# Performance work log

Hardware: AMD Instinct MI355X
Metric: run time of the kernel (lower is better)

Reference implementation:

```python
import jax, jax.numpy as jnp
import numpy as np

H = 8      # heads
D = 64     # dim_head
N0 = 1024  # modality-0 tokens
N1 = 1024  # modality-1 tokens
N = N0 + N1  # == token_num
DI = H * D   # dim_inner = 512


def setup_inputs() -> dict:
    key = jax.random.key(0)
    ks = jax.random.split(key, 10)
    s = 0.02
    return {
        "x0": jax.random.normal(ks[0], (1, N0, 512), jnp.float32),
        "x1": jax.random.normal(ks[1], (1, N1, 512), jnp.float32),
        "mask0": jnp.ones((1, N0), jnp.bool_),
        "mask1": jnp.ones((1, N1), jnp.bool_),
        "attn_dist": jax.random.normal(ks[2], (1, N, N), jnp.float32),
        "W_in0": jax.random.normal(ks[3], (512, 3 * DI), jnp.float32) * s,
        "W_in1": jax.random.normal(ks[4], (512, 3 * DI), jnp.float32) * s,
        "W_tau": jax.random.normal(ks[5], (DI, N * H), jnp.float32) * s,
        "b_tau": jax.random.normal(ks[6], (N * H,), jnp.float32) * s,
        "W_out0": jax.random.normal(ks[7], (DI, 512), jnp.float32) * s,
        "W_out1": jax.random.normal(ks[8], (DI, 512), jnp.float32) * s,
    }


def _split_heads(qkv, B, n):
    # (B, n, 3*H*D) -> (3, B, H, n, D)   [matches Rearrange 'b n (qkv h d) -> qkv b h n d']
    return qkv.reshape(B, n, 3, H, D).transpose(2, 0, 3, 1, 4)


def reference(x0, x1, mask0, mask1, attn_dist, W_in0, W_in1, W_tau, b_tau, W_out0, W_out1):
    B = x0.shape[0]
    qkv0 = _split_heads(x0 @ W_in0, B, N0)
    qkv1 = _split_heads(x1 @ W_in1, B, N1)
    qkv = jnp.concatenate([qkv0, qkv1], axis=3)  # pack along token axis -> (3,B,H,N,D)
    q, k, v = qkv[0], qkv[1], qkv[2]
    mask = jnp.concatenate([mask0, mask1], axis=1)  # (B, N)

    sim = jnp.einsum('bhid,bhjd->bhij', q, k) / jnp.sqrt(jnp.array(D, q.dtype))
    neg = -jnp.finfo(sim.dtype).max
    sim = jnp.where(mask[:, None, None, :], sim, neg)

    # taus: raw row-major reshape of q (B,H,N,D) -> (B,N,H*D), as in torch .reshape
    q_flat = q.reshape(B, N, H * D)
    taus = (q_flat @ W_tau + b_tau).reshape(B, N, N, H)
    bias = (taus * attn_dist[..., None]).transpose(0, 3, 1, 2)  # (B,H,N,N)
    sim = sim - bias

    attn = jax.nn.softmax(sim.astype(jnp.float32), axis=-1).astype(sim.dtype)
    out = jnp.einsum('bhij,bhjd->bhid', attn, v)
    out = out.transpose(0, 2, 1, 3).reshape(B, N, H * D)  # merge heads

    out0 = out[:, :N0] @ W_out0
    out1 = out[:, N0:] @ W_out1
    return (out0, out1)
```

## Files before the change

kernel.cpp:

```cpp
#include <hip/hip_runtime.h>
#include <stdint.h>

typedef __bf16 bf16;
typedef __bf16 bf16x8 __attribute__((ext_vector_type(8)));
typedef float f32x4 __attribute__((ext_vector_type(4)));
typedef unsigned short u16x8 __attribute__((ext_vector_type(8)));

#define MFMA16(a, b, c) __builtin_amdgcn_mfma_f32_16x16x32_bf16(a, b, c, 0, 0, 0)

static __device__ __forceinline__ bf16x8 lds_frag(const unsigned short* p) {
  return __builtin_bit_cast(bf16x8, *(const u16x8*)p);
}

static __device__ __forceinline__ u16x8 cvt8(const float* p) {
  f32x4 a = *(const f32x4*)p;
  f32x4 b = *(const f32x4*)(p + 4);
  u16x8 r;
#pragma unroll
  for (int e = 0; e < 4; ++e) {
    r[e] = __builtin_bit_cast(unsigned short, (bf16)a[e]);
    r[4 + e] = __builtin_bit_cast(unsigned short, (bf16)b[e]);
  }
  return r;
}

__global__ __launch_bounds__(256) void prep_kernel(
    const float* __restrict__ Wti, const float* __restrict__ btau,
    const float* __restrict__ x0, const float* __restrict__ x1,
    const float* __restrict__ Win0, const float* __restrict__ Win1,
    const float* __restrict__ Wo0, const float* __restrict__ Wo1,
    bf16* __restrict__ Wto, float* __restrict__ bto, bf16* __restrict__ xb,
    bf16* __restrict__ Winb0, bf16* __restrict__ Winb1,
    bf16* __restrict__ Wob0, bf16* __restrict__ Wob1) {
  const int b = blockIdx.x;
  const int tid = threadIdx.x;
  __shared__ unsigned short shm[8 * 32 * 72];

  if (b < 512) {
    const int c0 = (b & 7) * 64;
    const int j0 = (b >> 3) * 32;
#pragma unroll
    for (int it = 0; it < 8; ++it) {
      int idx = it * 256 + tid;
      int c = idx >> 5, j = idx & 31;
      u16x8 v = cvt8(Wti + (size_t)(c0 + c) * 16384 + (j0 + j) * 8);
#pragma unroll
      for (int h = 0; h < 8; ++h) shm[(h * 32 + j) * 72 + c] = v[h];
    }
    __syncthreads();
#pragma unroll
    for (int it = 0; it < 8; ++it) {
      int chunk = it * 256 + tid;
      int row = chunk >> 3, ck = chunk & 7;
      int h = row >> 5, j = row & 31;
      u16x8 v = *(const u16x8*)&shm[row * 72 + ck * 8];
      *(u16x8*)((unsigned short*)Wto + (size_t)(h * 2048 + j0 + j) * 512 + c0 + ck * 8) = v;
    }
    if ((b & 7) == 0) {
      int j = tid >> 3, h = tid & 7;
      bto[h * 2048 + j0 + j] = btau[(j0 + j) * 8 + h];
    }
  } else if (b < 896) {
    int t = b - 512;
    const float* W = t < 192 ? Win0 : Win1;
    bf16* Wb = t < 192 ? Winb0 : Winb1;
    t = t < 192 ? t : t - 192;
    const int c0 = (t & 7) * 64, n0 = (t >> 3) * 64;
#pragma unroll
    for (int it = 0; it < 2; ++it) {
      int idx = it * 256 + tid;
      int c = idx >> 3, nn = idx & 7;
      u16x8 v = cvt8(W + (size_t)(c0 + c) * 1536 + n0 + nn * 8);
#pragma unroll
      for (int e = 0; e < 8; ++e) shm[(nn * 8 + e) * 72 + c] = v[e];
    }
    __syncthreads();
#pragma unroll
    for (int it = 0; it < 2; ++it) {
      int idx = it * 256 + tid;
      int n = idx >> 3, ck = idx & 7;
      *(u16x8*)((unsigned short*)Wb + (size_t)(n0 + n) * 512 + c0 + ck * 8) =
          *(const u16x8*)&shm[n * 72 + ck * 8];
    }
  } else if (b < 1408) {
    int t = b - 896;
    const float* src = t < 256 ? x0 : x1;
    size_t dst0 = t < 256 ? 0 : 524288;
    int tt = t < 256 ? t : t - 256;
    size_t off = (size_t)tt * 2048 + tid * 8;
    u16x8 v = cvt8(src + off);
    *(u16x8*)((unsigned short*)xb + dst0 + off) = v;
  } else {
    int t = b - 1408;
    const float* W = t < 64 ? Wo0 : Wo1;
    bf16* Wb = t < 64 ? Wob0 : Wob1;
    t &= 63;
    const int c0 = (t & 7) * 64, n0 = (t >> 3) * 64;
#pragma unroll
    for (int it = 0; it < 2; ++it) {
      int idx = it * 256 + tid;
      int c = idx >> 3, nn = idx & 7;
      u16x8 v = cvt8(W + (size_t)(c0 + c) * 512 + n0 + nn * 8);
#pragma unroll
      for (int e = 0; e < 8; ++e) shm[(nn * 8 + e) * 72 + c] = v[e];
    }
    __syncthreads();
#pragma unroll
    for (int it = 0; it < 2; ++it) {
      int idx = it * 256 + tid;
      int n = idx >> 3, ck = idx & 7;
      *(u16x8*)((unsigned short*)Wb + (size_t)(n0 + n) * 512 + c0 + ck * 8) =
          *(const u16x8*)&shm[n * 72 + ck * 8];
    }
  }
}

__global__ __launch_bounds__(256) void qkv_gemm(
    const bf16* __restrict__ xb, const bf16* __restrict__ Winb0, const bf16* __restrict__ Winb1,
    bf16* __restrict__ Qb, bf16* __restrict__ Kb, bf16* __restrict__ Vb) {
  const int i0 = blockIdx.x * 128, c0 = blockIdx.y * 128;
  const bf16* Bm = (i0 < 1024) ? Winb0 : Winb1;
  const int tid = threadIdx.x;
  const int lane = tid & 63, wave = tid >> 6;
  const int l16 = lane & 15, quad = lane >> 4;
  const int mrow = (wave & 1) * 64, ncol = (wave >> 1) * 64;
  __shared__ unsigned short As[128 * 64];
  __shared__ unsigned short Bs[128 * 64];
  f32x4 acc[4][4] = {};

  for (int k0 = 0; k0 < 512; k0 += 64) {
    __syncthreads();
#pragma unroll
    for (int c = 0; c < 4; ++c) {
      int s = c * 256 + tid;
      int row = s >> 3, pos = s & 7;
      int kc = pos ^ (row & 7);
      __builtin_amdgcn_global_load_lds((const unsigned int*)(xb + (size_t)(i0 + row) * 512 + k0 + kc * 8),
                                       (unsigned int*)&As[s * 8], 16, 0, 0);
      __builtin_amdgcn_global_load_lds((const unsigned int*)(Bm + (size_t)(c0 + row) * 512 + k0 + kc * 8),
                                       (unsigned int*)&Bs[s * 8], 16, 0, 0);
    }
    __syncthreads();
#pragma unroll
    for (int kb = 0; kb < 2; ++kb) {
      bf16x8 a[4], b[4];
#pragma unroll
      for (int mt = 0; mt < 4; ++mt) {
        int row = mrow + mt * 16 + l16;
        a[mt] = lds_frag(&As[row * 64 + (((kb * 4 + quad) ^ (row & 7)) * 8)]);
      }
#pragma unroll
      for (int nt = 0; nt < 4; ++nt) {
        int row = ncol + nt * 16 + l16;
        b[nt] = lds_frag(&Bs[row * 64 + (((kb * 4 + quad) ^ (row & 7)) * 8)]);
      }
#pragma unroll
      for (int mt = 0; mt < 4; ++mt)
#pragma unroll
        for (int nt = 0; nt < 4; ++nt) acc[mt][nt] = MFMA16(a[mt], b[nt], acc[mt][nt]);
    }
  }
#pragma unroll
  for (int mt = 0; mt < 4; ++mt)
#pragma unroll
    for (int nt = 0; nt < 4; ++nt)
#pragma unroll
      for (int r = 0; r < 4; ++r) {
        int row = i0 + mrow + mt * 16 + quad * 4 + r;
        int col = c0 + ncol + nt * 16 + l16;
        int qsel = col >> 9, h = (col >> 6) & 7, d = col & 63;
        bf16* dst = qsel == 0 ? Qb : (qsel == 1 ? Kb : Vb);
        dst[(size_t)(h * 2048 + row) * 64 + d] = (bf16)acc[mt][nt][r];
      }
}

__global__ __launch_bounds__(256) void tau_gemm(
    const bf16* __restrict__ Qb, const bf16* __restrict__ Wt,
    const float* __restrict__ bt, const float* __restrict__ ad, bf16* __restrict__ T) {
  const int i0 = blockIdx.x * 128;
  const int j0 = blockIdx.y * 16;
  const int tid = threadIdx.x;
  const int lane = tid & 63, wave = tid >> 6;
  const int l16 = lane & 15, quad = lane >> 4;
  const int mrow = (wave & 1) * 64, ncol = (wave >> 1) * 64;
  __shared__ unsigned short As[128 * 128];
  __shared__ unsigned short Bs[128 * 128];
  f32x4 acc[4][4] = {};

  for (int k0 = 0; k0 < 512; k0 += 128) {
    __syncthreads();
#pragma unroll
    for (int c = 0; c < 8; ++c) {
      int s = c * 256 + tid;
      int row = s >> 4, pos = s & 15;
      int kc = pos ^ (row & 7);
      __builtin_amdgcn_global_load_lds((const unsigned int*)(Qb + (size_t)(i0 + row) * 512 + k0 + kc * 8),
                                       (unsigned int*)&As[s * 8], 16, 0, 0);
      __builtin_amdgcn_global_load_lds(
          (const unsigned int*)(Wt + (size_t)((row >> 4) * 2048 + j0 + (row & 15)) * 512 + k0 + kc * 8),
          (unsigned int*)&Bs[s * 8], 16, 0, 0);
    }
    __syncthreads();
#pragma unroll
    for (int kb = 0; kb < 4; ++kb) {
      bf16x8 a[4], b[4];
#pragma unroll
      for (int mt = 0; mt < 4; ++mt) {
        int row = mrow + mt * 16 + l16;
        a[mt] = lds_frag(&As[row * 128 + (((kb * 4 + quad) ^ (row & 7)) * 8)]);
      }
#pragma unroll
      for (int nt = 0; nt < 4; ++nt) {
        int row = ncol + nt * 16 + l16;
        b[nt] = lds_frag(&Bs[row * 128 + (((kb * 4 + quad) ^ (row & 7)) * 8)]);
      }
#pragma unroll
      for (int mt = 0; mt < 4; ++mt)
#pragma unroll
        for (int nt = 0; nt < 4; ++nt) acc[mt][nt] = MFMA16(a[mt], b[nt], acc[mt][nt]);
    }
  }
  float btv[4];
  int hh[4];
#pragma unroll
  for (int nt = 0; nt < 4; ++nt) {
    int c = ncol + nt * 16 + l16;
    hh[nt] = c >> 4;
    btv[nt] = bt[hh[nt] * 2048 + j0 + l16];
  }
#pragma unroll
  for (int mt = 0; mt < 4; ++mt)
#pragma unroll
    for (int r = 0; r < 4; ++r) {
      int row = i0 + mrow + mt * 16 + quad * 4 + r;
      float av = ad[(size_t)row * 2048 + j0 + l16];
#pragma unroll
      for (int nt = 0; nt < 4; ++nt)
        T[(size_t)hh[nt] * 4194304 + (size_t)row * 2048 + j0 + l16] =
            (bf16)((acc[mt][nt][r] + btv[nt]) * av);
    }
}

__global__ __launch_bounds__(256) void attn_kernel(
    const bf16* __restrict__ Qb, const bf16* __restrict__ Kb, const bf16* __restrict__ Vb,
    const bf16* __restrict__ T, float* __restrict__ Op, float* __restrict__ Ml) {
  const int h = blockIdx.y;
  const int i0 = blockIdx.x * 64;
  const int js = blockIdx.z;
  const int tid = threadIdx.x;
  const int lane = tid & 63, wave = tid >> 6;
  const int l16 = lane & 15, quad = lane >> 4;
  __shared__ unsigned short Ks[64 * 72];
  __shared__ unsigned short Vt[64 * 72];
  __shared__ unsigned short Ps[64 * 72];
  __shared__ unsigned short Tb[64 * 64];

  bf16x8 aQ[2];
#pragma unroll
  for (int kk = 0; kk < 2; ++kk)
    aQ[kk] = __builtin_bit_cast(
        bf16x8, *(const u16x8*)((const unsigned short*)Qb +
                                (size_t)(h * 2048 + i0 + wave * 16 + l16) * 64 + kk * 32 + quad * 8));
  f32x4 Oacc[4] = {};
  float m_run[4], l_run[4];
#pragma unroll
  for (int r = 0; r < 4; ++r) { m_run[r] = -3.0e38f; l_run[r] = 0.f; }
  const bf16* Th = T + (size_t)h * (2048 * 2048);

  for (int t = 0; t < 8; ++t) {
    const int j0 = js * 512 + t * 64;
    u16x8 vk[2], vv[2];
#pragma unroll
    for (int c = 0; c < 2; ++c) {
      int s = c * 256 + tid;
      int row = s >> 3, dc = s & 7;
      vk[c] = *(const u16x8*)((const unsigned short*)Kb + (size_t)(h * 2048 + j0 + row) * 64 + dc * 8);
      vv[c] = *(const u16x8*)((const unsigned short*)Vb + (size_t)(h * 2048 + j0 + row) * 64 + dc * 8);
    }
    __syncthreads();
#pragma unroll
    for (int c = 0; c < 2; ++c) {
      int s = c * 256 + tid;
      __builtin_amdgcn_global_load_lds(
          (const unsigned int*)(Th + (size_t)(i0 + (s >> 3)) * 2048 + j0 + (s & 7) * 8),
          (unsigned int*)&Tb[s * 8], 16, 0, 0);
      int row = s >> 3, dc = s & 7;
      *(u16x8*)&Ks[row * 72 + dc * 8] = vk[c];
#pragma unroll
      for (int e = 0; e < 8; ++e) Vt[(dc * 8 + e) * 72 + row] = vv[c][e];
    }
    __syncthreads();

    f32x4 S[4] = {};
#pragma unroll
    for (int nt = 0; nt < 4; ++nt)
#pragma unroll
      for (int kk = 0; kk < 2; ++kk) {
        bf16x8 bk = lds_frag(&Ks[(nt * 16 + l16) * 72 + kk * 32 + quad * 8]);
        S[nt] = MFMA16(aQ[kk], bk, S[nt]);
      }
    float sv[4][4];
#pragma unroll
    for (int nt = 0; nt < 4; ++nt)
#pragma unroll
      for (int r = 0; r < 4; ++r) {
        float tb = (float)__builtin_bit_cast(
            bf16, Tb[(wave * 16 + quad * 4 + r) * 64 + nt * 16 + l16]);
        sv[nt][r] = S[nt][r] * 0.125f - tb;
      }
#pragma unroll
    for (int r = 0; r < 4; ++r) {
      float mx = fmaxf(fmaxf(sv[0][r], sv[1][r]), fmaxf(sv[2][r], sv[3][r]));
#pragma unroll
      for (int o = 1; o < 16; o <<= 1) mx = fmaxf(mx, __shfl_xor(mx, o, 16));
      float mnew = fmaxf(m_run[r], mx);
      float alpha = __expf(m_run[r] - mnew);
      m_run[r] = mnew;
      float rs = 0.f;
#pragma unroll
      for (int nt = 0; nt < 4; ++nt) { sv[nt][r] = __expf(sv[nt][r] - mnew); rs += sv[nt][r]; }
#pragma unroll
      for (int o = 1; o < 16; o <<= 1) rs += __shfl_xor(rs, o, 16);
      l_run[r] = l_run[r] * alpha + rs;
#pragma unroll
      for (int dt = 0; dt < 4; ++dt) Oacc[dt][r] *= alpha;
    }
#pragma unroll
    for (int nt = 0; nt < 4; ++nt)
#pragma unroll
      for (int r = 0; r < 4; ++r)
        Ps[(wave * 16 + quad * 4 + r) * 72 + nt * 16 + l16] =
            __builtin_bit_cast(unsigned short, (bf16)sv[nt][r]);
    __syncthreads();
#pragma unroll
    for (int kk = 0; kk < 2; ++kk) {
      bf16x8 aP = lds_frag(&Ps[(wave * 16 + l16) * 72 + kk * 32 + quad * 8]);
#pragma unroll
      for (int dt = 0; dt < 4; ++dt) {
        bf16x8 bv = lds_frag(&Vt[(dt * 16 + l16) * 72 + kk * 32 + quad * 8]);
        Oacc[dt] = MFMA16(aP, bv, Oacc[dt]);
      }
    }
  }
  const size_t pb = ((size_t)js * 8 + h) * 2048;
#pragma unroll
  for (int r = 0; r < 4; ++r) {
    int rowg = i0 + wave * 16 + quad * 4 + r;
#pragma unroll
    for (int dt = 0; dt < 4; ++dt)
      Op[(pb + rowg) * 64 + dt * 16 + l16] = Oacc[dt][r];
    if (l16 == 0) {
      Ml[(pb + rowg) * 2 + 0] = m_run[r];
      Ml[(pb + rowg) * 2 + 1] = l_run[r];
    }
  }
}

__global__ __launch_bounds__(256) void merge_kernel(
    const float* __restrict__ Op, const float* __restrict__ Ml, bf16* __restrict__ om) {
  const int gr = blockIdx.x * 4 + (threadIdx.x >> 6);
  const int d = threadIdx.x & 63;
  float ms[4];
  float mmax = -3.0e38f;
#pragma unroll
  for (int s = 0; s < 4; ++s) {
    ms[s] = Ml[((size_t)s * 16384 + gr) * 2 + 0];
    mmax = fmaxf(mmax, ms[s]);
  }
  float lsum = 0.f, o = 0.f;
#pragma unroll
  for (int s = 0; s < 4; ++s) {
    float w = __expf(ms[s] - mmax);
    lsum += Ml[((size_t)s * 16384 + gr) * 2 + 1] * w;
    o += Op[((size_t)s * 16384 + gr) * 64 + d] * w;
  }
  int h = gr >> 11, i = gr & 2047;
  om[(size_t)i * 512 + h * 64 + d] = (bf16)(o / lsum);
}

__global__ __launch_bounds__(256) void out_proj(
    const bf16* __restrict__ om, const bf16* __restrict__ Wob0, const bf16* __restrict__ Wob1,
    float* __restrict__ out) {
  const int mod = blockIdx.z;
  const bf16* Bw = mod ? Wob1 : Wob0;
  float* outp = out + (size_t)mod * (1024 * 512);
  const int i0 = blockIdx.x * 64, c0 = blockIdx.y * 64;
  const int grow0 = mod * 1024 + i0;
  const int tid = threadIdx.x;
  const int lane = tid & 63, wave = tid >> 6;
  const int l16 = lane & 15, quad = lane >> 4;
  const int mrow = (wave & 1) * 32, ncol = (wave >> 1) * 32;
  __shared__ unsigned short As[64 * 64];
  __shared__ unsigned short Bs[64 * 64];
  f32x4 acc[2][2] = {};

  for (int k0 = 0; k0 < 512; k0 += 64) {
    __syncthreads();
#pragma unroll
    for (int c = 0; c < 2; ++c) {
      int s = c * 256 + tid;
      int row = s >> 3, pos = s & 7;
      int kc = pos ^ (row & 7);
      __builtin_amdgcn_global_load_lds((const unsigned int*)(om + (size_t)(grow0 + row) * 512 + k0 + kc * 8),
                                       (unsigned int*)&As[s * 8], 16, 0, 0);
      __builtin_amdgcn_global_load_lds((const unsigned int*)(Bw + (size_t)(c0 + row) * 512 + k0 + kc * 8),
                                       (unsigned int*)&Bs[s * 8], 16, 0, 0);
    }
    __syncthreads();
#pragma unroll
    for (int kb = 0; kb < 2; ++kb) {
      bf16x8 a[2], b[2];
#pragma unroll
      for (int mt = 0; mt < 2; ++mt) {
        int row = mrow + mt * 16 + l16;
        a[mt] = lds_frag(&As[row * 64 + (((kb * 4 + quad) ^ (row & 7)) * 8)]);
      }
#pragma unroll
      for (int nt = 0; nt < 2; ++nt) {
        int row = ncol + nt * 16 + l16;
        b[nt] = lds_frag(&Bs[row * 64 + (((kb * 4 + quad) ^ (row & 7)) * 8)]);
      }
#pragma unroll
      for (int mt = 0; mt < 2; ++mt)
#pragma unroll
        for (int nt = 0; nt < 2; ++nt) acc[mt][nt] = MFMA16(a[mt], b[nt], acc[mt][nt]);
    }
  }
#pragma unroll
  for (int mt = 0; mt < 2; ++mt)
#pragma unroll
    for (int nt = 0; nt < 2; ++nt)
#pragma unroll
      for (int r = 0; r < 4; ++r) {
        int row = i0 + mrow + mt * 16 + quad * 4 + r;
        int col = c0 + ncol + nt * 16 + l16;
        outp[(size_t)row * 512 + col] = acc[mt][nt][r];
      }
}

extern "C" void kernel_launch(void* const* d_in, const int* in_sizes, int n_in,
                              void* d_out, int out_size, void* d_ws, size_t ws_size,
                              hipStream_t stream) {
  (void)in_sizes; (void)n_in; (void)out_size; (void)ws_size;
  const float* x0   = (const float*)d_in[0];
  const float* x1   = (const float*)d_in[1];
  const float* ad   = (const float*)d_in[4];
  const float* Win0 = (const float*)d_in[5];
  const float* Win1 = (const float*)d_in[6];
  const float* Wtau = (const float*)d_in[7];
  const float* btau = (const float*)d_in[8];
  const float* Wo0  = (const float*)d_in[9];
  const float* Wo1  = (const float*)d_in[10];
  float* out = (float*)d_out;

  bf16* ws = (bf16*)d_ws;
  bf16* Qb = ws;
  bf16* Kb = Qb + 1048576;
  bf16* Vb = Kb + 1048576;
  bf16* Wt = Vb + 1048576;
  bf16* T  = Wt + 8388608;
  bf16* om = T + 33554432;
  float* bt = (float*)(om + 1048576);
  float* Ml = bt + 16384;
  bf16* Wob0 = (bf16*)(Ml + 131072);
  bf16* Wob1 = Wob0 + 262144;
  float* Op = (float*)Wt;
  bf16* xb    = T;
  bf16* Winb0 = T + 1048576;
  bf16* Winb1 = Winb0 + 786432;

  prep_kernel<<<1536, 256, 0, stream>>>(Wtau, btau, x0, x1, Win0, Win1, Wo0, Wo1,
                                        Wt, bt, xb, Winb0, Winb1, Wob0, Wob1);
  qkv_gemm<<<dim3(16, 12), 256, 0, stream>>>(xb, Winb0, Winb1, Qb, Kb, Vb);
  tau_gemm<<<dim3(16, 128), 256, 0, stream>>>(Qb, Wt, bt, ad, T);
  attn_kernel<<<dim3(32, 8, 4), 256, 0, stream>>>(Qb, Kb, Vb, T, Op, Ml);
  merge_kernel<<<4096, 256, 0, stream>>>(Op, Ml, om);
  out_proj<<<dim3(16, 8, 2), 256, 0, stream>>>(om, Wob0, Wob1, out);
}
```

Baseline: 242.3 us.

## Load K, V and tau-bias fragments directly from global memory in attention

The QKV GEMM now writes V transposed (head, dim, token) so the attention kernel can read MFMA B-fragments for K and V straight from global memory instead of staging them through LDS. The tau bias is also read per lane from global rather than via an async LDS copy, and the two block-wide barriers per tile become a wave-local wait and barrier around the private P staging. This removes LDS staging and block synchronisation at the cost of redundant global/L2 traffic, since each wave now fetches the same K/V tiles, and the scattered transposed V store in the QKV GEMM is uncoalesced.

```diff
diff --git a/kernel.cpp b/kernel.cpp
--- a/kernel.cpp
+++ b/kernel.cpp
@@ -9,6 +9,10 @@
 #define MFMA16(a, b, c) __builtin_amdgcn_mfma_f32_16x16x32_bf16(a, b, c, 0, 0, 0)
 
 static __device__ __forceinline__ bf16x8 lds_frag(const unsigned short* p) {
+  return __builtin_bit_cast(bf16x8, *(const u16x8*)p);
+}
+
+static __device__ __forceinline__ bf16x8 gmem_frag(const bf16* p) {
   return __builtin_bit_cast(bf16x8, *(const u16x8*)p);
 }
 
@@ -117,7 +121,7 @@
 
 __global__ __launch_bounds__(256) void qkv_gemm(
     const bf16* __restrict__ xb, const bf16* __restrict__ Winb0, const bf16* __restrict__ Winb1,
-    bf16* __restrict__ Qb, bf16* __restrict__ Kb, bf16* __restrict__ Vb) {
+    bf16* __restrict__ Qb, bf16* __restrict__ Kb, bf16* __restrict__ Vt_g) {
   const int i0 = blockIdx.x * 128, c0 = blockIdx.y * 128;
   const bf16* Bm = (i0 < 1024) ? Winb0 : Winb1;
   const int tid = threadIdx.x;
@@ -169,8 +173,13 @@
         int row = i0 + mrow + mt * 16 + quad * 4 + r;
         int col = c0 + ncol + nt * 16 + l16;
         int qsel = col >> 9, h = (col >> 6) & 7, d = col & 63;
-        bf16* dst = qsel == 0 ? Qb : (qsel == 1 ? Kb : Vb);
-        dst[(size_t)(h * 2048 + row) * 64 + d] = (bf16)acc[mt][nt][r];
+        bf16 val = (bf16)acc[mt][nt][r];
+        if (qsel == 2) {
+          Vt_g[(size_t)(h * 64 + d) * 2048 + row] = val;
+        } else {
+          bf16* dst = qsel == 0 ? Qb : Kb;
+          dst[(size_t)(h * 2048 + row) * 64 + d] = val;
+        }
       }
 }
 
@@ -242,7 +251,7 @@
 }
 
 __global__ __launch_bounds__(256) void attn_kernel(
-    const bf16* __restrict__ Qb, const bf16* __restrict__ Kb, const bf16* __restrict__ Vb,
+    const bf16* __restrict__ Qb, const bf16* __restrict__ Kb, const bf16* __restrict__ Vt_g,
     const bf16* __restrict__ T, float* __restrict__ Op, float* __restrict__ Ml) {
   const int h = blockIdx.y;
   const int i0 = blockIdx.x * 64;
@@ -250,64 +259,50 @@
   const int tid = threadIdx.x;
   const int lane = tid & 63, wave = tid >> 6;
   const int l16 = lane & 15, quad = lane >> 4;
-  __shared__ unsigned short Ks[64 * 72];
-  __shared__ unsigned short Vt[64 * 72];
   __shared__ unsigned short Ps[64 * 72];
-  __shared__ unsigned short Tb[64 * 64];
+
+  const bf16* Kh = Kb + (size_t)h * (2048 * 64);
+  const bf16* Vh = Vt_g + (size_t)h * (64 * 2048);
+  const bf16* Th = T + (size_t)h * (2048 * 2048);
 
   bf16x8 aQ[2];
 #pragma unroll
   for (int kk = 0; kk < 2; ++kk)
-    aQ[kk] = __builtin_bit_cast(
-        bf16x8, *(const u16x8*)((const unsigned short*)Qb +
-                                (size_t)(h * 2048 + i0 + wave * 16 + l16) * 64 + kk * 32 + quad * 8));
+    aQ[kk] = gmem_frag(Qb + (size_t)(h * 2048 + i0 + wave * 16 + l16) * 64 + kk * 32 + quad * 8);
   f32x4 Oacc[4] = {};
   float m_run[4], l_run[4];
 #pragma unroll
   for (int r = 0; r < 4; ++r) { m_run[r] = -3.0e38f; l_run[r] = 0.f; }
-  const bf16* Th = T + (size_t)h * (2048 * 2048);
+  const int rowl = wave * 16 + quad * 4;
 
   for (int t = 0; t < 8; ++t) {
     const int j0 = js * 512 + t * 64;
-    u16x8 vk[2], vv[2];
-#pragma unroll
-    for (int c = 0; c < 2; ++c) {
-      int s = c * 256 + tid;
-      int row = s >> 3, dc = s & 7;
-      vk[c] = *(const u16x8*)((const unsigned short*)Kb + (size_t)(h * 2048 + j0 + row) * 64 + dc * 8);
-      vv[c] = *(const u16x8*)((const unsigned short*)Vb + (size_t)(h * 2048 + j0 + row) * 64 + dc * 8);
-    }
-    __syncthreads();
-#pragma unroll
-    for (int c = 0; c < 2; ++c) {
-      int s = c * 256 + tid;
-      __builtin_amdgcn_global_load_lds(
-          (const unsigned int*)(Th + (size_t)(i0 + (s >> 3)) * 2048 + j0 + (s & 7) * 8),
-          (unsigned int*)&Tb[s * 8], 16, 0, 0);
-      int row = s >> 3, dc = s & 7;
-      *(u16x8*)&Ks[row * 72 + dc * 8] = vk[c];
-#pragma unroll
-      for (int e = 0; e < 8; ++e) Vt[(dc * 8 + e) * 72 + row] = vv[c][e];
-    }
-    __syncthreads();
+    bf16x8 bk[4][2];
+#pragma unroll
+    for (int nt = 0; nt < 4; ++nt)
+#pragma unroll
+      for (int kk = 0; kk < 2; ++kk)
+        bk[nt][kk] = gmem_frag(Kh + (size_t)(j0 + nt * 16 + l16) * 64 + kk * 32 + quad * 8);
+    unsigned short tbu[4][4];
+#pragma unroll
+    for (int nt = 0; nt < 4; ++nt)
+#pragma unroll
+      for (int r = 0; r < 4; ++r)
+        tbu[nt][r] = *((const unsigned short*)Th + (size_t)(i0 + rowl + r) * 2048 + j0 + nt * 16 + l16);
 
     f32x4 S[4] = {};
 #pragma unroll
     for (int nt = 0; nt < 4; ++nt)
 #pragma unroll
-      for (int kk = 0; kk < 2; ++kk) {
-        bf16x8 bk = lds_frag(&Ks[(nt * 16 + l16) * 72 + kk * 32 + quad * 8]);
-        S[nt] = MFMA16(aQ[kk], bk, S[nt]);
-      }
+      for (int kk = 0; kk < 2; ++kk) S[nt] = MFMA16(aQ[kk], bk[nt][kk], S[nt]);
+
     float sv[4][4];
 #pragma unroll
     for (int nt = 0; nt < 4; ++nt)
 #pragma unroll
-      for (int r = 0; r < 4; ++r) {
-        float tb = (float)__builtin_bit_cast(
-            bf16, Tb[(wave * 16 + quad * 4 + r) * 64 + nt * 16 + l16]);
-        sv[nt][r] = S[nt][r] * 0.125f - tb;
-      }
+      for (int r = 0; r < 4; ++r)
+        sv[nt][r] = S[nt][r] * 0.125f - (float)__builtin_bit_cast(bf16, tbu[nt][r]);
+
 #pragma unroll
     for (int r = 0; r < 4; ++r) {
       float mx = fmaxf(fmaxf(sv[0][r], sv[1][r]), fmaxf(sv[2][r], sv[3][r]));
@@ -329,23 +324,25 @@
     for (int nt = 0; nt < 4; ++nt)
 #pragma unroll
       for (int r = 0; r < 4; ++r)
-        Ps[(wave * 16 + quad * 4 + r) * 72 + nt * 16 + l16] =
+        Ps[(rowl + r) * 72 + nt * 16 + l16] =
             __builtin_bit_cast(unsigned short, (bf16)sv[nt][r]);
-    __syncthreads();
+    __builtin_amdgcn_s_waitcnt(0xC07F);
+    __builtin_amdgcn_wave_barrier();
 #pragma unroll
     for (int kk = 0; kk < 2; ++kk) {
       bf16x8 aP = lds_frag(&Ps[(wave * 16 + l16) * 72 + kk * 32 + quad * 8]);
 #pragma unroll
       for (int dt = 0; dt < 4; ++dt) {
-        bf16x8 bv = lds_frag(&Vt[(dt * 16 + l16) * 72 + kk * 32 + quad * 8]);
+        bf16x8 bv = gmem_frag(Vh + (size_t)(dt * 16 + l16) * 2048 + j0 + kk * 32 + quad * 8);
         Oacc[dt] = MFMA16(aP, bv, Oacc[dt]);
       }
     }
+    __builtin_amdgcn_wave_barrier();
   }
   const size_t pb = ((size_t)js * 8 + h) * 2048;
 #pragma unroll
   for (int r = 0; r < 4; ++r) {
-    int rowg = i0 + wave * 16 + quad * 4 + r;
+    int rowg = i0 + rowl + r;
 #pragma unroll
     for (int dt = 0; dt < 4; ++dt)
       Op[(pb + rowg) * 64 + dt * 16 + l16] = Oacc[dt][r];
@@ -456,8 +453,8 @@
   bf16* ws = (bf16*)d_ws;
   bf16* Qb = ws;
   bf16* Kb = Qb + 1048576;
-  bf16* Vb = Kb + 1048576;
-  bf16* Wt = Vb + 1048576;
+  bf16* Vt_g = Kb + 1048576;
+  bf16* Wt = Vt_g + 1048576;
   bf16* T  = Wt + 8388608;
   bf16* om = T + 33554432;
   float* bt = (float*)(om + 1048576);
@@ -471,9 +468,9 @@
 
   prep_kernel<<<1536, 256, 0, stream>>>(Wtau, btau, x0, x1, Win0, Win1, Wo0, Wo1,
                                         Wt, bt, xb, Winb0, Winb1, Wob0, Wob1);
-  qkv_gemm<<<dim3(16, 12), 256, 0, stream>>>(xb, Winb0, Winb1, Qb, Kb, Vb);
+  qkv_gemm<<<dim3(16, 12), 256, 0, stream>>>(xb, Winb0, Winb1, Qb, Kb, Vt_g);
   tau_gemm<<<dim3(16, 128), 256, 0, stream>>>(Qb, Wt, bt, ad, T);
-  attn_kernel<<<dim3(32, 8, 4), 256, 0, stream>>>(Qb, Kb, Vb, T, Op, Ml);
+  attn_kernel<<<dim3(32, 8, 4), 256, 0, stream>>>(Qb, Kb, Vt_g, T, Op, Ml);
   merge_kernel<<<4096, 256, 0, stream>>>(Op, Ml, om);
   out_proj<<<dim3(16, 8, 2), 256, 0, stream>>>(om, Wob0, Wob1, out);
 }
```

Result: slower. 263.8 us (+8.8%).
